# Kernel optimization log

Hardware: AMD Instinct MI355X
Metric: run time of the kernel (lower is better)

Reference implementation:

```python
import jax, jax.numpy as jnp
import numpy as np

B, S, D, H = 2, 2048, 2048, 16
DH = D // H


def setup_inputs() -> dict:
    key = jax.random.key(0)
    k1, k2, k3 = jax.random.split(key, 3)
    x = jax.random.normal(k1, (B, S, D), dtype=jnp.float32)
    Wqkv = jax.random.normal(k2, (D, 3 * D), dtype=jnp.float32) * (1.0 / np.sqrt(D))
    bqkv = jnp.zeros((3 * D,), dtype=jnp.float32)
    Wproj = jax.random.normal(k3, (D, D), dtype=jnp.float32) * (1.0 / np.sqrt(D))
    bproj = jnp.zeros((D,), dtype=jnp.float32)
    return {"x": x, "Wqkv": Wqkv, "bqkv": bqkv, "Wproj": Wproj, "bproj": bproj}


def reference(x, Wqkv, bqkv, Wproj, bproj):
    b, s, d = x.shape
    h, dh = H, DH
    # fused qkv projection: [b, s, 3, h, dh]
    qkv = (x @ Wqkv + bqkv).reshape(b, s, 3, h, dh)
    q, k, v = qkv[:, :, 0], qkv[:, :, 1], qkv[:, :, 2]  # each [b, s, h, dh]
    scale = 1.0 / np.sqrt(dh).astype(np.float32)
    # scores [b, h, q, k]
    attn = jnp.einsum('bqhd,bkhd->bhqk', q, k) * scale
    causal = jnp.tril(jnp.ones((s, s), dtype=bool))  # [s, s]
    attn = jnp.where(causal[None, None], attn, -jnp.inf)
    attn = jax.nn.softmax(attn, axis=-1)
    out = jnp.einsum('bhqk,bkhd->bqhd', attn, v).reshape(b, s, d)
    return out @ Wproj + bproj
```

## Files before the change

### kernel.cpp

```cpp
#include <hip/hip_runtime.h>
#include <hip/hip_bf16.h>

#define BB 2
#define SS 2048
#define DD 2048
#define HH 16
#define DHH 128
#define MM 4096
#define NN1 6144
#define NTILES (DD / 64)

typedef __attribute__((ext_vector_type(8))) short bf16x8;
typedef __attribute__((ext_vector_type(4))) float f32x4;
typedef unsigned int u32;

static __device__ __forceinline__ float exp2_hw(float x) {
  return __builtin_amdgcn_exp2f(x);
}

static __device__ __forceinline__ unsigned short f2bf(float f) {
  union { float f; u32 u; } v; v.f = f;
  return (unsigned short)((v.u + 0x7FFFu + ((v.u >> 16) & 1u)) >> 16);
}

static __device__ __forceinline__ void gload_lds16(const void* g, void* l) {
  __builtin_amdgcn_global_load_lds((const __attribute__((address_space(1))) u32*)g,
                                   (__attribute__((address_space(3))) u32*)l, 16, 0, 0);
}

__global__ __launch_bounds__(256) void k_cvt(const float* __restrict__ in,
                                             unsigned short* __restrict__ out) {
  int i = blockIdx.x * 256 + threadIdx.x;
  float4 v = ((const float4*)in)[i];
  ushort4 o;
  o.x = f2bf(v.x); o.y = f2bf(v.y); o.z = f2bf(v.z); o.w = f2bf(v.w);
  ((ushort4*)out)[i] = o;
}

__global__ __launch_bounds__(256) void k_transpose(const float* __restrict__ in,
                                                   unsigned short* __restrict__ out,
                                                   int R, int C) {
  __shared__ float t[32][33];
  int bx = blockIdx.x * 32, by = blockIdx.y * 32;
  int tx = threadIdx.x, ty = threadIdx.y;
  #pragma unroll
  for (int i = ty; i < 32; i += 8)
    t[i][tx] = in[(size_t)(by + i) * C + bx + tx];
  __syncthreads();
  #pragma unroll
  for (int i = ty; i < 32; i += 8)
    out[(size_t)(bx + i) * R + by + tx] = f2bf(t[tx][i]);
}

__device__ __forceinline__ void gemm_core(const char* __restrict__ Ag,
                                          const char* __restrict__ Bg,
                                          char* Alds, char* Blds,
                                          f32x4 acc[4][4]) {
  const int tid = threadIdx.x;
  const int wave = tid >> 6, lane = tid & 63;
  const int g = lane >> 4, c = lane & 15;
  const int wm = wave >> 1, wn = wave & 1;

  auto stageA = [&](int buf, int kt) {
    #pragma unroll
    for (int q = 0; q < 4; ++q) {
      int off = q * 8192 + wave * 1024 + (lane << 4);
      int row = off >> 7, cb = off & 127;
      gload_lds16(Ag + (size_t)row * 4096 + kt * 128 + (cb ^ ((row & 7) << 4)),
                  Alds + buf * 32768 + q * 8192 + wave * 1024);
    }
  };
  auto stageB = [&](int buf, int kt) {
    #pragma unroll
    for (int q = 0; q < 2; ++q) {
      int off = q * 8192 + wave * 1024 + (lane << 4);
      int row = off >> 7, cb = off & 127;
      gload_lds16(Bg + (size_t)row * 4096 + kt * 128 + (cb ^ ((row & 7) << 4)),
                  Blds + buf * 16384 + q * 8192 + wave * 1024);
    }
  };

  stageA(0, 0); stageB(0, 0);
  stageA(1, 1); stageB(1, 1);
  asm volatile("s_waitcnt vmcnt(6)" ::: "memory");
  __builtin_amdgcn_sched_barrier(0);
  __builtin_amdgcn_s_barrier();

  for (int t = 0; t < NTILES; ++t) {
    const int buf = t % 3;
    const char* Ab = Alds + buf * 32768;
    const char* Bb = Blds + buf * 16384;
    bf16x8 af[4][2], bfv[4][2];
    #pragma unroll
    for (int i = 0; i < 4; ++i) {
      int row = wm * 64 + i * 16 + c;
      af[i][0] = *(const bf16x8*)(Ab + row * 128 + ((g * 16) ^ ((row & 7) << 4)));
    }
    #pragma unroll
    for (int j = 0; j < 4; ++j) {
      int row = wn * 64 + j * 16 + c;
      bfv[j][0] = *(const bf16x8*)(Bb + row * 128 + ((g * 16) ^ ((row & 7) << 4)));
    }
    __builtin_amdgcn_sched_barrier(0);
    #pragma unroll
    for (int i = 0; i < 4; ++i) {
      int row = wm * 64 + i * 16 + c;
      af[i][1] = *(const bf16x8*)(Ab + row * 128 + ((64 + g * 16) ^ ((row & 7) << 4)));
    }
    #pragma unroll
    for (int j = 0; j < 4; ++j) {
      int row = wn * 64 + j * 16 + c;
      bfv[j][1] = *(const bf16x8*)(Bb + row * 128 + ((64 + g * 16) ^ ((row & 7) << 4)));
    }
    if (t + 2 < NTILES) {
      int nb = buf + 2; if (nb >= 3) nb -= 3;
      stageA(nb, t + 2);
      stageB(nb, t + 2);
    }
    asm volatile("s_waitcnt lgkmcnt(8)" ::: "memory");
    __builtin_amdgcn_sched_barrier(0);
    __builtin_amdgcn_s_setprio(1);
    #pragma unroll
    for (int i = 0; i < 4; ++i)
      #pragma unroll
      for (int j = 0; j < 4; ++j)
        acc[i][j] = __builtin_amdgcn_mfma_f32_16x16x32_bf16(af[i][0], bfv[j][0], acc[i][j], 0, 0, 0);
    __builtin_amdgcn_s_setprio(0);
    asm volatile("s_waitcnt lgkmcnt(0)" ::: "memory");
    __builtin_amdgcn_sched_barrier(0);
    __builtin_amdgcn_s_setprio(1);
    #pragma unroll
    for (int i = 0; i < 4; ++i)
      #pragma unroll
      for (int j = 0; j < 4; ++j)
        acc[i][j] = __builtin_amdgcn_mfma_f32_16x16x32_bf16(af[i][1], bfv[j][1], acc[i][j], 0, 0, 0);
    __builtin_amdgcn_s_setprio(0);
    if (t < NTILES - 1) {
      if (t + 2 < NTILES) { asm volatile("s_waitcnt vmcnt(6)" ::: "memory"); }
      else                { asm volatile("s_waitcnt vmcnt(0)" ::: "memory"); }
      __builtin_amdgcn_sched_barrier(0);
      __builtin_amdgcn_s_barrier();
    }
  }
}

__global__ __launch_bounds__(512, 1) void k_gemm1(const unsigned short* __restrict__ A,
                                                  const unsigned short* __restrict__ Bt,
                                                  const float* __restrict__ bias,
                                                  unsigned short* __restrict__ Qb,
                                                  unsigned short* __restrict__ Kb,
                                                  unsigned short* __restrict__ Vt) {
  __shared__ __align__(16) char lds[147456];
  const int n0 = blockIdx.x * 128, m0 = blockIdx.y * 256;
  f32x4 acc[4][4] = {};
  gemm_core((const char*)A + (size_t)m0 * 4096,
            (const char*)Bt + (size_t)n0 * 4096,
            lds, lds + 98304, acc);
  const int lane = threadIdx.x & 63, wave = threadIdx.x >> 6;
  const int g = lane >> 4, c = lane & 15;
  const int wm = wave >> 1, wn = wave & 1;
  const int head = (n0 >> 7) & 15, which = n0 >> 11;
  const float qsc = 0.12751879523263566f;
  #pragma unroll
  for (int i = 0; i < 4; ++i) {
    int rowb = m0 + wm * 64 + i * 16 + g * 4;
    int bb = rowb >> 11, s = rowb & 2047;
    #pragma unroll
    for (int j = 0; j < 4; ++j) {
      int dh = wn * 64 + j * 16 + c;
      float bv = bias[n0 + dh];
      if (which == 2) {
        ushort4 p;
        p.x = f2bf(acc[i][j][0] + bv);
        p.y = f2bf(acc[i][j][1] + bv);
        p.z = f2bf(acc[i][j][2] + bv);
        p.w = f2bf(acc[i][j][3] + bv);
        *(ushort4*)(Vt + ((size_t)(bb * HH + head) * DHH + dh) * SS + s) = p;
      } else {
        float v0 = acc[i][j][0] + bv, v1 = acc[i][j][1] + bv;
        float v2 = acc[i][j][2] + bv, v3 = acc[i][j][3] + bv;
        if (which == 0) { v0 *= qsc; v1 *= qsc; v2 *= qsc; v3 *= qsc; }
        unsigned short* dst = (which == 0 ? Qb : Kb) + ((size_t)(bb * HH + head) * SS + s) * DHH + dh;
        dst[0]       = f2bf(v0);
        dst[DHH]     = f2bf(v1);
        dst[2 * DHH] = f2bf(v2);
        dst[3 * DHH] = f2bf(v3);
      }
    }
  }
}

__global__ __launch_bounds__(512, 1) void k_gemm2(const unsigned short* __restrict__ A,
                                                  const unsigned short* __restrict__ Bt,
                                                  const float* __restrict__ bias,
                                                  float* __restrict__ out) {
  __shared__ __align__(16) char lds[147456];
  const int n0 = blockIdx.x * 128, m0 = blockIdx.y * 256;
  f32x4 acc[4][4] = {};
  gemm_core((const char*)A + (size_t)m0 * 4096,
            (const char*)Bt + (size_t)n0 * 4096,
            lds, lds + 98304, acc);
  const int lane = threadIdx.x & 63, wave = threadIdx.x >> 6;
  const int g = lane >> 4, c = lane & 15;
  const int wm = wave >> 1, wn = wave & 1;
  #pragma unroll
  for (int i = 0; i < 4; ++i) {
    int rowb = m0 + wm * 64 + i * 16 + g * 4;
    #pragma unroll
    for (int j = 0; j < 4; ++j) {
      int gcol = n0 + wn * 64 + j * 16 + c;
      float bv = bias[gcol];
      #pragma unroll
      for (int r = 0; r < 4; ++r)
        out[(size_t)(rowb + r) * DD + gcol] = acc[i][j][r] + bv;
    }
  }
}

__global__ __launch_bounds__(256, 2) void k_attn(const unsigned short* __restrict__ Qb,
                                                 const unsigned short* __restrict__ Kb,
                                                 const unsigned short* __restrict__ Vt,
                                                 unsigned short* __restrict__ O) {
  __shared__ __align__(16) unsigned short Kt[2][64 * 128];
  __shared__ __align__(16) unsigned short Vs[2][128 * 64];
  __shared__ __align__(16) unsigned short Pl[4][32 * 64];
  const int qtl = (blockIdx.y < 16) ? blockIdx.x : (15 - blockIdx.x);
  const int bh = blockIdx.y;
  const int b = bh >> 4, h = bh & 15;
  const int tid = threadIdx.x, wave = tid >> 6, lane = tid & 63;
  const int g = lane >> 4, c = lane & 15;
  const int q0w = qtl * 128 + wave * 32;
  const unsigned short* Qp = Qb + (size_t)bh * SS * DHH;
  const unsigned short* Kp = Kb + (size_t)bh * SS * DHH;
  const unsigned short* Vp = Vt + (size_t)bh * DHH * SS;

  bf16x8 qf[2][4];
  #pragma unroll
  for (int m = 0; m < 2; ++m)
    #pragma unroll
    for (int ks = 0; ks < 4; ++ks)
      qf[m][ks] = *(const bf16x8*)(Qp + (size_t)(q0w + m * 16 + c) * DHH + ks * 32 + g * 8);

  f32x4 acc[2][8] = {};
  float lsum[2] = {0.f, 0.f};

  auto stage = [&](int buf, int kv0) {
    #pragma unroll
    for (int r = 0; r < 4; ++r) {
      int base = r * 4096 + wave * 1024;
      int off = base + (lane << 4);
      { int row = off >> 8; int cb = (off & 255) ^ ((row & 7) << 4);
        gload_lds16((const char*)Kp + (size_t)(kv0 + row) * 256 + cb,
                    (char*)Kt[buf] + base); }
      { int row = off >> 7; int cb = (off & 127) ^ ((row & 7) << 4);
        gload_lds16((const char*)Vp + (size_t)row * (SS * 2) + (size_t)kv0 * 2 + cb,
                    (char*)Vs[buf] + base); }
    }
  };

  const int ntiles = 2 * qtl + 2;
  stage(0, 0);
  __syncthreads();

  for (int t = 0; t < ntiles; ++t) {
    const int cur = t & 1;
    const int kv0 = t * 64;
    if (t + 1 < ntiles) stage(cur ^ 1, kv0 + 64);
    if (kv0 <= q0w + 31) {
      const unsigned short* K_ = Kt[cur];
      const unsigned short* V_ = Vs[cur];
      f32x4 sa[2][4] = {};
      __builtin_amdgcn_s_setprio(1);
      #pragma unroll
      for (int nb = 0; nb < 4; ++nb) {
        const int rk = nb * 16 + c;
        const int swz = (rk & 7) << 4;
        #pragma unroll
        for (int ks = 0; ks < 4; ++ks) {
          bf16x8 kf = *(const bf16x8*)((const char*)K_ + rk * 256 + ((ks * 64 + g * 16) ^ swz));
          sa[0][nb] = __builtin_amdgcn_mfma_f32_16x16x32_bf16(kf, qf[0][ks], sa[0][nb], 0, 0, 0);
          sa[1][nb] = __builtin_amdgcn_mfma_f32_16x16x32_bf16(kf, qf[1][ks], sa[1][nb], 0, 0, 0);
        }
      }
      __builtin_amdgcn_s_setprio(0);
      const bool diag = (kv0 + 63 > q0w);
      #pragma unroll
      for (int m = 0; m < 2; ++m) {
        const int q = q0w + m * 16 + c;
        float p[4][4];
        float rs = 0.f;
        if (diag) {
          #pragma unroll
          for (int nb = 0; nb < 4; ++nb)
            #pragma unroll
            for (int r = 0; r < 4; ++r) {
              float s = (kv0 + nb * 16 + g * 4 + r > q) ? -1e30f : sa[m][nb][r];
              p[nb][r] = exp2_hw(s);
              rs += p[nb][r];
            }
        } else {
          #pragma unroll
          for (int nb = 0; nb < 4; ++nb)
            #pragma unroll
            for (int r = 0; r < 4; ++r) {
              p[nb][r] = exp2_hw(sa[m][nb][r]);
              rs += p[nb][r];
            }
        }
        rs += __shfl_xor(rs, 16, 64);
        rs += __shfl_xor(rs, 32, 64);
        lsum[m] += rs;
        const int rowp = m * 16 + c;
        const int swzp = (rowp & 7) << 4;
        #pragma unroll
        for (int nb = 0; nb < 4; ++nb)
          #pragma unroll
          for (int i2 = 0; i2 < 2; ++i2) {
            u32 w = (u32)f2bf(p[nb][2 * i2]) | ((u32)f2bf(p[nb][2 * i2 + 1]) << 16);
            *(u32*)((char*)Pl[wave] + rowp * 128 + (((nb * 16 + g * 4 + 2 * i2) * 2) ^ swzp)) = w;
          }
      }
      asm volatile("s_waitcnt lgkmcnt(0)" ::: "memory");
      __builtin_amdgcn_sched_barrier(0);
      bf16x8 pf[2][2];
      #pragma unroll
      for (int m = 0; m < 2; ++m)
        #pragma unroll
        for (int c2 = 0; c2 < 2; ++c2) {
          int rowp = m * 16 + c;
          pf[m][c2] = *(const bf16x8*)((const char*)Pl[wave] + rowp * 128 +
                                       ((c2 * 64 + g * 16) ^ ((rowp & 7) << 4)));
        }
      __builtin_amdgcn_s_setprio(1);
      #pragma unroll
      for (int nf = 0; nf < 8; ++nf) {
        const int rv = nf * 16 + c;
        const int swzv = (rv & 7) << 4;
        #pragma unroll
        for (int c2 = 0; c2 < 2; ++c2) {
          bf16x8 vf = *(const bf16x8*)((const char*)V_ + rv * 128 + ((c2 * 64 + g * 16) ^ swzv));
          acc[0][nf] = __builtin_amdgcn_mfma_f32_16x16x32_bf16(pf[0][c2], vf, acc[0][nf], 0, 0, 0);
          acc[1][nf] = __builtin_amdgcn_mfma_f32_16x16x32_bf16(pf[1][c2], vf, acc[1][nf], 0, 0, 0);
        }
      }
      __builtin_amdgcn_s_setprio(0);
    }
    __syncthreads();
  }

  unsigned short* Op = O + (size_t)b * SS * DD + (size_t)h * DHH;
  #pragma unroll
  for (int m = 0; m < 2; ++m) {
    float inv = 1.0f / lsum[m];
    float invr[4];
    #pragma unroll
    for (int r = 0; r < 4; ++r)
      invr[r] = __shfl(inv, 20 * g + r, 64);
    #pragma unroll
    for (int nf = 0; nf < 8; ++nf)
      #pragma unroll
      for (int r = 0; r < 4; ++r) {
        int q = q0w + m * 16 + g * 4 + r;
        Op[(size_t)q * DD + nf * 16 + c] = f2bf(acc[m][nf][r] * invr[r]);
      }
  }
}

extern "C" void kernel_launch(void* const* d_in, const int* in_sizes, int n_in,
                              void* d_out, int out_size, void* d_ws, size_t ws_size,
                              hipStream_t stream) {
  const float* x     = (const float*)d_in[0];
  const float* Wqkv  = (const float*)d_in[1];
  const float* bqkv  = (const float*)d_in[2];
  const float* Wproj = (const float*)d_in[3];
  const float* bproj = (const float*)d_in[4];
  float* out = (float*)d_out;

  char* ws = (char*)d_ws;
  unsigned short* xb  = (unsigned short*)ws; ws += (size_t)MM * DD * 2;
  unsigned short* w1t = (unsigned short*)ws; ws += (size_t)NN1 * DD * 2;
  unsigned short* w2t = (unsigned short*)ws; ws += (size_t)DD * DD * 2;
  unsigned short* Qb  = (unsigned short*)ws; ws += (size_t)BB * HH * SS * DHH * 2;
  unsigned short* Kb  = (unsigned short*)ws; ws += (size_t)BB * HH * SS * DHH * 2;
  unsigned short* Vt  = (unsigned short*)ws; ws += (size_t)BB * HH * SS * DHH * 2;
  unsigned short* Ob  = (unsigned short*)ws; ws += (size_t)MM * DD * 2;

  k_cvt<<<dim3((MM * DD) / 1024), 256, 0, stream>>>(x, xb);
  k_transpose<<<dim3(NN1 / 32, DD / 32), dim3(32, 8), 0, stream>>>(Wqkv, w1t, DD, NN1);
  k_transpose<<<dim3(DD / 32, DD / 32), dim3(32, 8), 0, stream>>>(Wproj, w2t, DD, DD);
  k_gemm1<<<dim3(NN1 / 128, MM / 256), 512, 0, stream>>>(xb, w1t, bqkv, Qb, Kb, Vt);
  k_attn<<<dim3(SS / 128, BB * HH), 256, 0, stream>>>(Qb, Kb, Vt, Ob);
  k_gemm2<<<dim3(DD / 128, MM / 256), 512, 0, stream>>>(Ob, w2t, bproj, out);
}
```

Baseline: 251.7 us.

## Retile QKV GEMM to 256x192 blocks with a 512-block grid and swizzled mapping

Replaces the 256x128 QKV GEMM tiling (768 blocks) with 256x192 tiles, so the grid is exactly 512 blocks, two per CU on a 256-CU device, and avoids a partial wave. Each wave now computes 128x48 with an 8x3 accumulator array. The block index is remapped so neighbouring blocks share A and B tiles for better L2 reuse. The new core uses double-buffered LDS with a full vmcnt(0) wait each iteration, which may expose more load latency than the old deeper pipeline. The epilogue now works out which of Q, K or V and which head per column, because 192-wide tiles cross head boundaries.

```diff
diff --git a/kernel.cpp b/kernel.cpp
--- a/kernel.cpp
+++ b/kernel.cpp
@@ -52,6 +52,89 @@
     out[(size_t)(bx + i) * R + by + tx] = f2bf(t[tx][i]);
 }
 
+__device__ __forceinline__ void gemm_core192(const char* __restrict__ Ag,
+                                             const char* __restrict__ Bg,
+                                             char* lds, f32x4 acc[8][3]) {
+  const int tid = threadIdx.x;
+  const int wave = tid >> 6, lane = tid & 63;
+  const int g = lane >> 4, c = lane & 15;
+  const int wm = wave >> 2, wn = wave & 3;
+
+  auto stage = [&](int buf, int kt) {
+    char* base = lds + buf * 57344;
+    #pragma unroll
+    for (int q = 0; q < 4; ++q) {
+      int off = q * 8192 + tid * 16;
+      int row = off >> 7, cb = off & 127;
+      gload_lds16(Ag + (size_t)row * 4096 + kt * 128 + (cb ^ ((row & 7) << 4)),
+                  base + q * 8192 + wave * 1024);
+    }
+    #pragma unroll
+    for (int q = 0; q < 3; ++q) {
+      int off = q * 8192 + tid * 16;
+      int row = off >> 7, cb = off & 127;
+      gload_lds16(Bg + (size_t)row * 4096 + kt * 128 + (cb ^ ((row & 7) << 4)),
+                  base + 32768 + q * 8192 + wave * 1024);
+    }
+  };
+
+  stage(0, 0);
+  asm volatile("s_waitcnt vmcnt(0)" ::: "memory");
+  __builtin_amdgcn_sched_barrier(0);
+  __builtin_amdgcn_s_barrier();
+
+  for (int t = 0; t < NTILES; ++t) {
+    const char* Ab = lds + (t & 1) * 57344;
+    const char* Bb = Ab + 32768;
+    bf16x8 af[8][2], bfv[3][2];
+    #pragma unroll
+    for (int i = 0; i < 8; ++i) {
+      int row = wm * 128 + i * 16 + c;
+      af[i][0] = *(const bf16x8*)(Ab + row * 128 + ((g * 16) ^ ((row & 7) << 4)));
+    }
+    #pragma unroll
+    for (int j = 0; j < 3; ++j) {
+      int row = wn * 48 + j * 16 + c;
+      bfv[j][0] = *(const bf16x8*)(Bb + row * 128 + ((g * 16) ^ ((row & 7) << 4)));
+    }
+    __builtin_amdgcn_sched_barrier(0);
+    #pragma unroll
+    for (int i = 0; i < 8; ++i) {
+      int row = wm * 128 + i * 16 + c;
+      af[i][1] = *(const bf16x8*)(Ab + row * 128 + ((64 + g * 16) ^ ((row & 7) << 4)));
+    }
+    #pragma unroll
+    for (int j = 0; j < 3; ++j) {
+      int row = wn * 48 + j * 16 + c;
+      bfv[j][1] = *(const bf16x8*)(Bb + row * 128 + ((64 + g * 16) ^ ((row & 7) << 4)));
+    }
+    if (t + 1 < NTILES) stage((t + 1) & 1, t + 1);
+    asm volatile("s_waitcnt lgkmcnt(11)" ::: "memory");
+    __builtin_amdgcn_sched_barrier(0);
+    __builtin_amdgcn_s_setprio(1);
+    #pragma unroll
+    for (int i = 0; i < 8; ++i)
+      #pragma unroll
+      for (int j = 0; j < 3; ++j)
+        acc[i][j] = __builtin_amdgcn_mfma_f32_16x16x32_bf16(af[i][0], bfv[j][0], acc[i][j], 0, 0, 0);
+    __builtin_amdgcn_s_setprio(0);
+    asm volatile("s_waitcnt lgkmcnt(0)" ::: "memory");
+    __builtin_amdgcn_sched_barrier(0);
+    __builtin_amdgcn_s_setprio(1);
+    #pragma unroll
+    for (int i = 0; i < 8; ++i)
+      #pragma unroll
+      for (int j = 0; j < 3; ++j)
+        acc[i][j] = __builtin_amdgcn_mfma_f32_16x16x32_bf16(af[i][1], bfv[j][1], acc[i][j], 0, 0, 0);
+    __builtin_amdgcn_s_setprio(0);
+    if (t < NTILES - 1) {
+      asm volatile("s_waitcnt vmcnt(0)" ::: "memory");
+      __builtin_amdgcn_sched_barrier(0);
+      __builtin_amdgcn_s_barrier();
+    }
+  }
+}
+
 __device__ __forceinline__ void gemm_core(const char* __restrict__ Ag,
                                           const char* __restrict__ Bg,
                                           char* Alds, char* Blds,
@@ -150,25 +233,28 @@
                                                   unsigned short* __restrict__ Qb,
                                                   unsigned short* __restrict__ Kb,
                                                   unsigned short* __restrict__ Vt) {
-  __shared__ __align__(16) char lds[147456];
-  const int n0 = blockIdx.x * 128, m0 = blockIdx.y * 256;
-  f32x4 acc[4][4] = {};
-  gemm_core((const char*)A + (size_t)m0 * 4096,
-            (const char*)Bt + (size_t)n0 * 4096,
-            lds, lds + 98304, acc);
+  __shared__ __align__(16) char lds[114688];
+  const int x = blockIdx.x & 7, k = blockIdx.x >> 3;
+  const int mt = (x & 1) * 8 + (k & 7), nt = (x >> 1) * 8 + (k >> 3);
+  const int m0 = mt * 256, n0 = nt * 192;
+  f32x4 acc[8][3] = {};
+  gemm_core192((const char*)A + (size_t)m0 * 4096,
+               (const char*)Bt + (size_t)n0 * 4096,
+               lds, acc);
   const int lane = threadIdx.x & 63, wave = threadIdx.x >> 6;
   const int g = lane >> 4, c = lane & 15;
-  const int wm = wave >> 1, wn = wave & 1;
-  const int head = (n0 >> 7) & 15, which = n0 >> 11;
+  const int wm = wave >> 2, wn = wave & 3;
   const float qsc = 0.12751879523263566f;
   #pragma unroll
-  for (int i = 0; i < 4; ++i) {
-    int rowb = m0 + wm * 64 + i * 16 + g * 4;
+  for (int i = 0; i < 8; ++i) {
+    int rowb = m0 + wm * 128 + i * 16 + g * 4;
     int bb = rowb >> 11, s = rowb & 2047;
     #pragma unroll
-    for (int j = 0; j < 4; ++j) {
-      int dh = wn * 64 + j * 16 + c;
-      float bv = bias[n0 + dh];
+    for (int j = 0; j < 3; ++j) {
+      int gcol = n0 + wn * 48 + j * 16 + c;
+      int which = gcol >> 11;
+      int head = (gcol >> 7) & 15, dh = gcol & 127;
+      float bv = bias[gcol];
       if (which == 2) {
         ushort4 p;
         p.x = f2bf(acc[i][j][0] + bv);
@@ -388,7 +474,7 @@
   k_cvt<<<dim3((MM * DD) / 1024), 256, 0, stream>>>(x, xb);
   k_transpose<<<dim3(NN1 / 32, DD / 32), dim3(32, 8), 0, stream>>>(Wqkv, w1t, DD, NN1);
   k_transpose<<<dim3(DD / 32, DD / 32), dim3(32, 8), 0, stream>>>(Wproj, w2t, DD, DD);
-  k_gemm1<<<dim3(NN1 / 128, MM / 256), 512, 0, stream>>>(xb, w1t, bqkv, Qb, Kb, Vt);
+  k_gemm1<<<dim3(512), 512, 0, stream>>>(xb, w1t, bqkv, Qb, Kb, Vt);
   k_attn<<<dim3(SS / 128, BB * HH), 256, 0, stream>>>(Qb, Kb, Vt, Ob);
   k_gemm2<<<dim3(DD / 128, MM / 256), 512, 0, stream>>>(Ob, w2t, bproj, out);
 }
```

Result: faster. 242.4 us (-3.7%).
